# Performance work log

Measured on AMD Instinct MI355X. Metric: run time of the kernel, lower is better.

## Reference

```python
import jax, jax.numpy as jnp
from jax import lax
import numpy as np

N, BITS, NCLS = 2048, 64, 100
LAMBDA = 1.0
ALPHA = 1.0


def setup_inputs() -> dict:
    key = jax.random.key(0)
    ku, kl = jax.random.split(key)
    u = jax.random.normal(ku, (N, BITS), dtype=jnp.float32)
    labels = jax.random.randint(kl, (N,), 0, NCLS)
    y = jax.nn.one_hot(labels, NCLS, dtype=jnp.float32)  # [N, C]
    return {"u": u, "y": y}


def reference(u, y):
    # inner_product[i, j] = <u_i, u_j>;  s[i, j] = (y_i . y_j > 0)
    ip = u @ u.T                      # [N, N]
    s = (y @ y.T) > 0                 # [N, N] bool

    def step(carry, xs):
        tot, cnt = carry
        ip_row, s_row = xs            # [N], [N]
        pos = s_row
        neg = ~s_row
        # triple[p, n] = ip[p] - ip[n] - ALPHA, clamped like the original
        T = jnp.clip(ip_row[:, None] - ip_row[None, :] - ALPHA, -100.0, 50.0)
        # -(T - log(1 + exp(T))) = softplus(T) - T
        L = jax.nn.softplus(T) - T    # [N, N]
        pm = (pos[:, None] & neg[None, :]).astype(L.dtype)
        npairs = pm.sum()
        valid = (pos.sum() > 0) & (neg.sum() > 0)
        row_loss = jnp.where(valid, (L * pm).sum() / jnp.maximum(npairs, 1.0), 0.0)
        return (tot + row_loss, cnt + valid.astype(jnp.float32)), None

    (tot, cnt), _ = lax.scan(step, (jnp.float32(0.0), jnp.float32(0.0)), (ip, s))
    loss1 = jnp.where(cnt > 0, tot / jnp.maximum(cnt, 1.0), 0.0)
    loss2 = LAMBDA * jnp.mean((u - jnp.sign(u)) ** 2)
    return loss1 + loss2
```

## Files before the change

kernel.cpp:

```cpp
#include <hip/hip_runtime.h>
#include <hip/hip_bf16.h>
#include <math.h>

#define NROWS 2048
#define BITS  64
#define NCLS  100
#define ALPHA_C  1.0f
#define LAMBDA_C 1.0f
#define ECLAMP   1.0e9f
#define NPMAX    64
#define EPS      20
#define NCHUNK   32

typedef __bf16 bf16x8 __attribute__((ext_vector_type(8)));
typedef float  floatx4 __attribute__((ext_vector_type(4)));


__device__ __forceinline__ float block_reduce_sum(float v, float* wsum) {
    __syncthreads();
    #pragma unroll
    for (int off = 32; off > 0; off >>= 1) v += __shfl_down(v, off);
    int tid = threadIdx.x;
    if ((tid & 63) == 0) wsum[tid >> 6] = v;
    __syncthreads();
    float r = 0.f;
    if (tid == 0) {
        #pragma unroll
        for (int w = 0; w < 4; ++w) r += wsum[w];
    }
    return r;
}

__device__ __forceinline__ float softplus_mt(float T) {
    return fmaxf(-T, 0.f) + __logf(1.f + __expf(-fabsf(T)));
}


__global__ __launch_bounds__(256) void prep_kernel(const float* __restrict__ u,
                                                   const float* __restrict__ y,
                                                   unsigned short* __restrict__ ub,
                                                   unsigned char* __restrict__ lab8,
                                                   float* __restrict__ qp,
                                                   float* __restrict__ rl,
                                                   unsigned int* __restrict__ done) {
    const int tid = threadIdx.x;
    if (blockIdx.x < 64) {
        __shared__ float wsum[4];
        const int base = blockIdx.x * 2048 + tid * 8;
        float4 v0 = *(const float4*)(u + base);
        float4 v1 = *(const float4*)(u + base + 4);
        float vv[8] = {v0.x, v0.y, v0.z, v0.w, v1.x, v1.y, v1.z, v1.w};
        unsigned short ob[8];
        float q = 0.f;
        #pragma unroll
        for (int m = 0; m < 8; ++m) {
            const float v = vv[m];
            const float sg = (v > 0.f) ? 1.f : ((v < 0.f) ? -1.f : 0.f);
            const float d = v - sg;
            q = fmaf(d, d, q);
            __hip_bfloat16 h = __float2bfloat16(v);
            ob[m] = *reinterpret_cast<unsigned short*>(&h);
        }
        *(uint4*)(ub + base) = *(const uint4*)ob;
        float t = block_reduce_sum(q, wsum);
        if (tid == 0) qp[blockIdx.x] = t;
    } else {
        const int bi = blockIdx.x - 64;
        if (bi == 0 && tid == 0) *done = 0u;
        if (tid == 0) ((float4*)rl)[bi] = make_float4(0.f, 0.f, 0.f, 0.f);
        const int row = bi * 4 + (tid >> 6);
        const int lane = tid & 63;
        const float* yr = y + (size_t)row * NCLS;
        float v0 = yr[lane];
        float v1 = (lane < NCLS - 64) ? yr[lane + 64] : 0.f;
        unsigned long long m0 = __ballot(v0 > 0.5f);
        unsigned long long m1 = __ballot(v1 > 0.5f);
        if (lane == 0) {
            int c = m0 ? (__ffsll(m0) - 1) : (m1 ? 64 + __ffsll(m1) - 1 : 0);
            lab8[row] = (unsigned char)c;
        }
    }
}

__global__ __launch_bounds__(512, 4) void fused_kernel(const float* __restrict__ u,
                                                       const unsigned short* __restrict__ ub,
                                                       const unsigned char* __restrict__ lab8,
                                                       const float* __restrict__ qp,
                                                       float* __restrict__ rl,
                                                       unsigned int* __restrict__ done,
                                                       float* __restrict__ out) {
    __shared__ unsigned char labL[NROWS];
    __shared__ float uloc[16][BITS];
    __shared__ float epT[NPMAX][EPS];
    __shared__ int   clsIdx[NROWS];
    __shared__ int   whist[NCHUNK][NCLS];
    __shared__ int   ccnt[NCLS];
    __shared__ int   cofs[NCLS];
    __shared__ int   np16[16];
    __shared__ float wsum[16][8];
    __shared__ float red8[8];
    __shared__ int   lastflag;

    const int tid  = threadIdx.x;
    const int wave = tid >> 6;
    const int lane = tid & 63;
    const int rsel = lane & 15;
    const int quad = lane >> 4;
    const int koff = quad * 8;
    const int i0    = (blockIdx.x >> 2) * 16;
    const int jbase = (blockIdx.x & 3) * 512;

    ((unsigned int*)labL)[tid] = ((const unsigned int*)lab8)[tid];
    {
        int* wf = &whist[0][0];
        #pragma unroll
        for (int k = 0; k < 7; ++k) {
            const int idx = tid + k * 512;
            if (idx < NCHUNK * NCLS) wf[idx] = 0;
        }
    }
    __syncthreads();

    int rk[4], rc[4];
    const unsigned long long below = (1ull << lane) - 1ull;
    #pragma unroll
    for (int s = 0; s < 4; ++s) {
        const int t = wave * 4 + s;
        const int c = labL[t * 64 + lane];
        unsigned long long m = ~0ull;
        #pragma unroll
        for (int b = 0; b < 7; ++b) {
            const unsigned long long bb = __ballot((c >> b) & 1);
            m &= ((c >> b) & 1) ? bb : ~bb;
        }
        rk[s] = (int)__popcll(m & below);
        rc[s] = c;
        whist[t][c] = (int)__popcll(m);
    }
    __syncthreads();

    if (tid < NCLS) {
        int run = 0;
        #pragma unroll
        for (int t = 0; t < NCHUNK; ++t) {
            const int v = whist[t][tid];
            whist[t][tid] = run;
            run += v;
        }
        ccnt[tid] = run;
    }
    __syncthreads();

    if (tid < 64) {
        const int c0 = (tid < 50) ? ccnt[2 * tid] : 0;
        const int c1 = (tid < 50) ? ccnt[2 * tid + 1] : 0;
        int p = c0 + c1;
        #pragma unroll
        for (int off = 1; off < 64; off <<= 1) {
            const int n = __shfl_up(p, off);
            if (tid >= off) p += n;
        }
        const int excl = p - (c0 + c1);
        if (tid < 50) { cofs[2 * tid] = excl; cofs[2 * tid + 1] = excl + c0; }
    }
    __syncthreads();

    #pragma unroll
    for (int s = 0; s < 4; ++s) {
        const int t = wave * 4 + s;
        const int c = rc[s];
        clsIdx[cofs[c] + whist[t][c] + rk[s]] = t * 64 + lane;
    }
    __syncthreads();

    {
        const int gr = tid >> 5;
        const int gp = tid & 31;
        const int grow = clsIdx[i0 + gr];
        ((float2*)&uloc[gr][0])[gp] =
            ((const float2*)(u + (size_t)grow * BITS))[gp];
    }
    const int arow = clsIdx[i0 + rsel];
    uint4 a0r = *(const uint4*)(ub + (size_t)arow * BITS + koff);
    uint4 a1r = *(const uint4*)(ub + (size_t)arow * BITS + 32 + koff);

    #pragma unroll
    for (int s2 = 0; s2 < 2; ++s2) {
        const int r16 = wave * 2 + s2;
        const int ci  = labL[clsIdx[i0 + r16]];
        const int np  = ccnt[ci];
        const int base = cofs[ci];
        const int npc = (np < NPMAX) ? np : NPMAX;
        float val = 0.f;
        if (lane < npc) {
            const int j = clsIdx[base + lane];
            const float4* uj4 = (const float4*)(u + (size_t)j * BITS);
            const float4* ui4 = (const float4*)(&uloc[r16][0]);
            float s0 = 0.f, s1 = 0.f, s2v = 0.f, s3 = 0.f;
            #pragma unroll
            for (int kk = 0; kk < BITS / 4; ++kk) {
                float4 vj = uj4[kk];
                float4 vi = ui4[kk];
                s0 = fmaf(vj.x, vi.x, s0);
                s1 = fmaf(vj.y, vi.y, s1);
                s2v = fmaf(vj.z, vi.z, s2v);
                s3 = fmaf(vj.w, vi.w, s3);
            }
            val = fminf(__expf(-((s0 + s1) + (s2v + s3))), ECLAMP);
        }
        epT[lane][r16] = val;
        if (lane == 0) np16[r16] = np;
    }

    int rlabq[4];
    #pragma unroll
    for (int r = 0; r < 4; ++r) rlabq[r] = labL[clsIdx[i0 + 4 * quad + r]];

    const bf16x8 A0 = __builtin_bit_cast(bf16x8, a0r);
    const bf16x8 A1 = __builtin_bit_cast(bf16x8, a1r);
    float Eb[4][4];
    #pragma unroll
    for (int t = 0; t < 4; ++t) {
        const int jr = jbase + (wave * 4 + t) * 16 + rsel;
        uint4 b0r = *(const uint4*)(ub + (size_t)jr * BITS + koff);
        uint4 b1r = *(const uint4*)(ub + (size_t)jr * BITS + 32 + koff);
        bf16x8 B0 = __builtin_bit_cast(bf16x8, b0r);
        bf16x8 B1 = __builtin_bit_cast(bf16x8, b1r);
        floatx4 cacc = {0.f, 0.f, 0.f, 0.f};
        cacc = __builtin_amdgcn_mfma_f32_16x16x32_bf16(A0, B0, cacc, 0, 0, 0);
        cacc = __builtin_amdgcn_mfma_f32_16x16x32_bf16(A1, B1, cacc, 0, 0, 0);
        const int colLab = labL[jr];
        #pragma unroll
        for (int r = 0; r < 4; ++r) {
            Eb[t][r] = (colLab == rlabq[r]) ? 0.f
                                            : fminf(__expf(cacc[r] + ALPHA_C), ECLAMP);
        }
    }
    __syncthreads();

    int npmx = 0;
    #pragma unroll
    for (int r = 0; r < 16; ++r) {
        int n = np16[r]; n = (n > NPMAX) ? NPMAX : n;
        npmx = (n > npmx) ? n : npmx;
    }
    const int npr4 = (npmx + 3) & ~3;

    const float SC = 0x1p-60f;
    float mprod[4] = {1.f, 1.f, 1.f, 1.f};
    int   eacc[4]  = {0, 0, 0, 0};
    for (int k = 0; k < npr4; k += 4) {
        const float4 e0 = *(const float4*)(&epT[k][4 * quad]);
        const float4 e1 = *(const float4*)(&epT[k + 1][4 * quad]);
        const float4 e2 = *(const float4*)(&epT[k + 2][4 * quad]);
        const float4 e3 = *(const float4*)(&epT[k + 3][4 * quad]);
        const float e0c[4] = {e0.x * SC, e0.y * SC, e0.z * SC, e0.w * SC};
        const float e1v[4] = {e1.x, e1.y, e1.z, e1.w};
        const float e2c[4] = {e2.x * SC, e2.y * SC, e2.z * SC, e2.w * SC};
        const float e3v[4] = {e3.x, e3.y, e3.z, e3.w};
        #pragma unroll
        for (int t = 0; t < 4; ++t) {
            #pragma unroll
            for (int r = 0; r < 4; ++r) {
                const float q0 = Eb[t][r];
                const float f0 = fmaf(q0, e0c[r], SC);
                const float f1 = fmaf(q0, e1v[r], 1.f);
                const float f2 = fmaf(q0, e2c[r], SC);
                const float f3 = fmaf(q0, e3v[r], 1.f);
                const float P  = (f0 * f1) * (f2 * f3);
                const unsigned int pb = __builtin_bit_cast(unsigned int, P);
                eacc[r] += (int)(pb >> 23);
                const float m = __builtin_bit_cast(float,
                                    (pb & 0x007FFFFFu) | 0x3F800000u);
                mprod[r] *= m;
            }
        }
    }
    const float nadj = 7.0f * (float)npr4;
    float s[4];
    #pragma unroll
    for (int r = 0; r < 4; ++r)
        s[r] = ((float)eacc[r] - nadj) + __log2f(mprod[r]);

    #pragma unroll
    for (int r = 0; r < 4; ++r) {
        #pragma unroll
        for (int off = 1; off < 16; off <<= 1) s[r] += __shfl_xor(s[r], off);
    }
    if (rsel == 0) {
        #pragma unroll
        for (int r = 0; r < 4; ++r) wsum[4 * quad + r][wave] = s[r];
    }
    __syncthreads();
    if (tid < 16) {
        const float ln2 = 0.6931471805599453f;
        const float tot = (((wsum[tid][0] + wsum[tid][1]) +
                            (wsum[tid][2] + wsum[tid][3])) +
                           ((wsum[tid][4] + wsum[tid][5]) +
                            (wsum[tid][6] + wsum[tid][7]))) * ln2;
        atomicAdd(&rl[clsIdx[i0 + tid]], tot);
    }
    __syncthreads();

    if (tid == 0) {
        __threadfence();
        const unsigned int old = atomicAdd(done, 1u);
        lastflag = (old == 511u) ? 1 : 0;
    }
    __syncthreads();
    if (lastflag) {
        float tsum = 0.f, vsum = 0.f;
        for (int row = tid; row < NROWS; row += 512) {
            const float rv = atomicAdd(&rl[row], 0.0f);
            const int np = ccnt[labL[row]];
            const int nn = NROWS - np;
            const int valid = (np > 0 && nn > 0) ? 1 : 0;
            tsum += valid ? (rv / fmaxf((float)np * (float)nn, 1.f)) : 0.f;
            vsum += (float)valid;
        }
        float q = (tid < 64) ? qp[tid] : 0.f;

        float vals[3] = {tsum, vsum, q};
        float outv[3];
        #pragma unroll
        for (int m = 0; m < 3; ++m) {
            float v = vals[m];
            #pragma unroll
            for (int off = 32; off > 0; off >>= 1) v += __shfl_down(v, off);
            if (lane == 0) red8[wave] = v;
            __syncthreads();
            float r = 0.f;
            if (tid == 0) {
                #pragma unroll
                for (int w = 0; w < 8; ++w) r += red8[w];
            }
            __syncthreads();
            outv[m] = r;
        }
        if (tid == 0) {
            const float loss1 = (outv[1] > 0.f) ? (outv[0] / fmaxf(outv[1], 1.f)) : 0.f;
            const float loss2 = LAMBDA_C * (outv[2] / (float)(NROWS * BITS));
            out[0] = loss1 + loss2;
        }
    }
}


__global__ __launch_bounds__(256) void labels_only_kernel(const float* __restrict__ y,
                                                          int* __restrict__ labels) {
    const int tid = threadIdx.x;
    const int row = blockIdx.x * 4 + (tid >> 6);
    const int lane = tid & 63;
    const float* yr = y + (size_t)row * NCLS;
    float v0 = yr[lane];
    float v1 = (lane < NCLS - 64) ? yr[lane + 64] : 0.f;
    unsigned long long m0 = __ballot(v0 > 0.5f);
    unsigned long long m1 = __ballot(v1 > 0.5f);
    if (lane == 0) {
        int c = m0 ? (__ffsll(m0) - 1) : (m1 ? 64 + __ffsll(m1) - 1 : 0);
        labels[row] = c;
    }
}

__global__ __launch_bounds__(256) void row_loss_kernel(const float* __restrict__ u,
                                                       const int* __restrict__ labels,
                                                       float* __restrict__ acc) {
    __shared__ float a[NROWS];
    __shared__ float apv[NROWS];
    __shared__ int lab[NROWS];
    __shared__ float ui[BITS];
    __shared__ int npos_s;
    __shared__ float wsum[4];

    const int i = blockIdx.x;
    const int tid = threadIdx.x;

    if (tid < BITS) ui[tid] = u[(size_t)i * BITS + tid];
    if (tid == 0) npos_s = 0;
    __syncthreads();

    #pragma unroll
    for (int m = 0; m < NROWS / 256; ++m) {
        const int j = tid + m * 256;
        const float4* uj = (const float4*)(u + (size_t)j * BITS);
        float s0 = 0.f, s1 = 0.f, s2 = 0.f, s3 = 0.f;
        #pragma unroll
        for (int q = 0; q < BITS / 4; ++q) {
            float4 v = uj[q];
            s0 = fmaf(v.x, ui[4 * q + 0], s0);
            s1 = fmaf(v.y, ui[4 * q + 1], s1);
            s2 = fmaf(v.z, ui[4 * q + 2], s2);
            s3 = fmaf(v.w, ui[4 * q + 3], s3);
        }
        a[j] = (s0 + s1) + (s2 + s3);
        lab[j] = labels[j];
    }
    __syncthreads();

    const int c = lab[i];
    #pragma unroll
    for (int m = 0; m < NROWS / 256; ++m) {
        const int j = tid + m * 256;
        if (lab[j] == c) { int k = atomicAdd(&npos_s, 1); apv[k] = a[j]; }
    }
    __syncthreads();
    const int npos = npos_s;
    const int nneg = NROWS - npos;

    float b[NROWS / 256];
    #pragma unroll
    for (int m = 0; m < NROWS / 256; ++m) {
        const int j = tid + m * 256;
        b[m] = (lab[j] != c) ? (a[j] + ALPHA_C) : -3.0e38f;
    }

    float lsum = 0.f;
    for (int k = 0; k < npos; ++k) {
        const float apk = apv[k];
        #pragma unroll
        for (int m = 0; m < NROWS / 256; ++m) lsum += softplus_mt(apk - b[m]);
    }

    float tot = block_reduce_sum(lsum, wsum);
    if (tid == 0) {
        const int valid = (npos > 0 && nneg > 0) ? 1 : 0;
        const float npairs = fmaxf((float)npos * (float)nneg, 1.f);
        const float rlv = valid ? (tot / npairs) : 0.f;
        atomicAdd(&acc[0], rlv);
        atomicAdd(&acc[1], (float)valid);
    }
}

__global__ __launch_bounds__(256) void quant_kernel(const float* __restrict__ u,
                                                    float* __restrict__ acc) {
    __shared__ float wsum[4];
    const int stride = gridDim.x * 256;
    float s = 0.f;
    for (int t = blockIdx.x * 256 + threadIdx.x; t < NROWS * BITS; t += stride) {
        float v = u[t];
        float sg = (v > 0.f) ? 1.f : ((v < 0.f) ? -1.f : 0.f);
        float d = v - sg;
        s = fmaf(d, d, s);
    }
    float tot = block_reduce_sum(s, wsum);
    if (threadIdx.x == 0) atomicAdd(&acc[2], tot);
}

__global__ void finalize_kernel(const float* __restrict__ acc,
                                float* __restrict__ out) {
    const float tot = acc[0], cnt = acc[1], q = acc[2];
    const float loss1 = (cnt > 0.f) ? (tot / fmaxf(cnt, 1.f)) : 0.f;
    const float loss2 = LAMBDA_C * (q / (float)(NROWS * BITS));
    out[0] = loss1 + loss2;
}


extern "C" void kernel_launch(void* const* d_in, const int* in_sizes, int n_in,
                              void* d_out, int out_size, void* d_ws, size_t ws_size,
                              hipStream_t stream) {
    const float* u = (const float*)d_in[0];
    const float* y = (const float*)d_in[1];
    float* out = (float*)d_out;

    unsigned char* lab8 = (unsigned char*)d_ws;
    unsigned int* done = (unsigned int*)((char*)d_ws + 4096);
    float* rl = (float*)((char*)d_ws + 8192);
    float* qp = (float*)((char*)d_ws + 16384);
    unsigned short* ub = (unsigned short*)((char*)d_ws + 24576);
    const size_t NEED = 24576 + (size_t)NROWS * BITS * sizeof(unsigned short);

    if (ws_size >= NEED) {
        prep_kernel<<<576, 256, 0, stream>>>(u, y, ub, lab8, qp, rl, done);
        fused_kernel<<<512, 512, 0, stream>>>(u, ub, lab8, qp, rl, done, out);
    } else {
        float* acc2 = (float*)d_ws;
        int*   lab2 = (int*)((char*)d_ws + 256);
        hipMemsetAsync(d_ws, 0, 256, stream);
        labels_only_kernel<<<512, 256, 0, stream>>>(y, lab2);
        row_loss_kernel<<<NROWS, 256, 0, stream>>>(u, lab2, acc2);
        quant_kernel<<<64, 256, 0, stream>>>(u, acc2);
        finalize_kernel<<<1, 1, 0, stream>>>(acc2, out);
    }
}
```

Measured before the change: 82.67 us.

## Hoist per-block class counting sort into a single separate sort kernel

Every fused block used to recompute the class histogram, prefix sums and sorted row index on its own. That work now runs once in a new single-block sortk_kernel, which writes a 16-bit sorted index plus class counts and offsets to workspace. The fused kernel just loads these into shared memory, which shrinks its LDS footprint and prologue. The cost is an extra kernel launch and a serial one-block step between prep and the fused kernel; the class-count scan is also reworked into parallel shuffle scans.

```diff
diff --git a/kernel.cpp b/kernel.cpp
--- a/kernel.cpp
+++ b/kernel.cpp
@@ -82,20 +82,105 @@
     }
 }
 
+__global__ __launch_bounds__(512) void sortk_kernel(const unsigned char* __restrict__ lab8,
+                                                    unsigned short* __restrict__ clsIdxG,
+                                                    int* __restrict__ ccntG,
+                                                    int* __restrict__ cofsG) {
+    __shared__ unsigned char labL[NROWS];
+    __shared__ int whist[NCHUNK][NCLS];
+    __shared__ int ccnt[NCLS];
+    __shared__ int cofs[NCLS];
+
+    const int tid  = threadIdx.x;
+    const int wave = tid >> 6;
+    const int lane = tid & 63;
+
+    ((unsigned int*)labL)[tid] = ((const unsigned int*)lab8)[tid];
+    {
+        int* wf = &whist[0][0];
+        #pragma unroll
+        for (int k = 0; k < 7; ++k) {
+            const int idx = tid + k * 512;
+            if (idx < NCHUNK * NCLS) wf[idx] = 0;
+        }
+    }
+    __syncthreads();
+
+    int rk[4], rc[4];
+    const unsigned long long below = (1ull << lane) - 1ull;
+    #pragma unroll
+    for (int s = 0; s < 4; ++s) {
+        const int t = wave * 4 + s;
+        const int c = labL[t * 64 + lane];
+        unsigned long long m = ~0ull;
+        #pragma unroll
+        for (int b = 0; b < 7; ++b) {
+            const unsigned long long bb = __ballot((c >> b) & 1);
+            m &= ((c >> b) & 1) ? bb : ~bb;
+        }
+        rk[s] = (int)__popcll(m & below);
+        rc[s] = c;
+        whist[t][c] = (int)__popcll(m);
+    }
+    __syncthreads();
+
+    #pragma unroll
+    for (int p = 0; p < 7; ++p) {
+        const int cls = p * 16 + (tid >> 5);
+        const int ch  = tid & 31;
+        if (cls < NCLS) {
+            const int v = whist[ch][cls];
+            int x = v;
+            #pragma unroll
+            for (int off = 1; off < 32; off <<= 1) {
+                const int n = __shfl_up(x, off, 32);
+                if (ch >= off) x += n;
+            }
+            whist[ch][cls] = x - v;
+            if (ch == 31) ccnt[cls] = x;
+        }
+    }
+    __syncthreads();
+
+    if (tid < 64) {
+        const int c0 = (tid < 50) ? ccnt[2 * tid] : 0;
+        const int c1 = (tid < 50) ? ccnt[2 * tid + 1] : 0;
+        int p = c0 + c1;
+        #pragma unroll
+        for (int off = 1; off < 64; off <<= 1) {
+            const int n = __shfl_up(p, off);
+            if (tid >= off) p += n;
+        }
+        const int excl = p - (c0 + c1);
+        if (tid < 50) { cofs[2 * tid] = excl; cofs[2 * tid + 1] = excl + c0; }
+    }
+    __syncthreads();
+
+    #pragma unroll
+    for (int s = 0; s < 4; ++s) {
+        const int t = wave * 4 + s;
+        const int c = rc[s];
+        clsIdxG[cofs[c] + whist[t][c] + rk[s]] = (unsigned short)(t * 64 + lane);
+    }
+    if (tid < NCLS) { ccntG[tid] = ccnt[tid]; cofsG[tid] = cofs[tid]; }
+}
+
 __global__ __launch_bounds__(512, 4) void fused_kernel(const float* __restrict__ u,
                                                        const unsigned short* __restrict__ ub,
                                                        const unsigned char* __restrict__ lab8,
+                                                       const unsigned short* __restrict__ clsIdxG,
+                                                       const int* __restrict__ ccntG,
+                                                       const int* __restrict__ cofsG,
                                                        const float* __restrict__ qp,
                                                        float* __restrict__ rl,
                                                        unsigned int* __restrict__ done,
                                                        float* __restrict__ out) {
     __shared__ unsigned char labL[NROWS];
+    __shared__ unsigned short clsL[NROWS];
     __shared__ float uloc[16][BITS];
     __shared__ float epT[NPMAX][EPS];
-    __shared__ int   clsIdx[NROWS];
-    __shared__ int   whist[NCHUNK][NCLS];
-    __shared__ int   ccnt[NCLS];
-    __shared__ int   cofs[NCLS];
+    __shared__ int   ccntL[NCLS];
+    __shared__ int   cofsL[NCLS];
     __shared__ int   np16[16];
     __shared__ float wsum[16][8];
     __shared__ float red8[8];
@@ -111,89 +196,31 @@
     const int jbase = (blockIdx.x & 3) * 512;
 
     ((unsigned int*)labL)[tid] = ((const unsigned int*)lab8)[tid];
-    {
-        int* wf = &whist[0][0];
-        #pragma unroll
-        for (int k = 0; k < 7; ++k) {
-            const int idx = tid + k * 512;
-            if (idx < NCHUNK * NCLS) wf[idx] = 0;
-        }
-    }
-    __syncthreads();
-
-    int rk[4], rc[4];
-    const unsigned long long below = (1ull << lane) - 1ull;
-    #pragma unroll
-    for (int s = 0; s < 4; ++s) {
-        const int t = wave * 4 + s;
-        const int c = labL[t * 64 + lane];
-        unsigned long long m = ~0ull;
-        #pragma unroll
-        for (int b = 0; b < 7; ++b) {
-            const unsigned long long bb = __ballot((c >> b) & 1);
-            m &= ((c >> b) & 1) ? bb : ~bb;
-        }
-        rk[s] = (int)__popcll(m & below);
-        rc[s] = c;
-        whist[t][c] = (int)__popcll(m);
-    }
-    __syncthreads();
-
-    if (tid < NCLS) {
-        int run = 0;
-        #pragma unroll
-        for (int t = 0; t < NCHUNK; ++t) {
-            const int v = whist[t][tid];
-            whist[t][tid] = run;
-            run += v;
-        }
-        ccnt[tid] = run;
-    }
-    __syncthreads();
-
-    if (tid < 64) {
-        const int c0 = (tid < 50) ? ccnt[2 * tid] : 0;
-        const int c1 = (tid < 50) ? ccnt[2 * tid + 1] : 0;
-        int p = c0 + c1;
-        #pragma unroll
-        for (int off = 1; off < 64; off <<= 1) {
-            const int n = __shfl_up(p, off);
-            if (tid >= off) p += n;
-        }
-        const int excl = p - (c0 + c1);
-        if (tid < 50) { cofs[2 * tid] = excl; cofs[2 * tid + 1] = excl + c0; }
-    }
-    __syncthreads();
-
-    #pragma unroll
-    for (int s = 0; s < 4; ++s) {
-        const int t = wave * 4 + s;
-        const int c = rc[s];
-        clsIdx[cofs[c] + whist[t][c] + rk[s]] = t * 64 + lane;
-    }
+    ((uint2*)clsL)[tid] = ((const uint2*)clsIdxG)[tid];
+    if (tid < NCLS) { ccntL[tid] = ccntG[tid]; cofsL[tid] = cofsG[tid]; }
     __syncthreads();
 
     {
         const int gr = tid >> 5;
         const int gp = tid & 31;
-        const int grow = clsIdx[i0 + gr];
+        const int grow = clsL[i0 + gr];
         ((float2*)&uloc[gr][0])[gp] =
             ((const float2*)(u + (size_t)grow * BITS))[gp];
     }
-    const int arow = clsIdx[i0 + rsel];
+    const int arow = clsL[i0 + rsel];
     uint4 a0r = *(const uint4*)(ub + (size_t)arow * BITS + koff);
     uint4 a1r = *(const uint4*)(ub + (size_t)arow * BITS + 32 + koff);
 
     #pragma unroll
     for (int s2 = 0; s2 < 2; ++s2) {
         const int r16 = wave * 2 + s2;
-        const int ci  = labL[clsIdx[i0 + r16]];
-        const int np  = ccnt[ci];
-        const int base = cofs[ci];
+        const int ci  = labL[clsL[i0 + r16]];
+        const int np  = ccntL[ci];
+        const int base = cofsL[ci];
         const int npc = (np < NPMAX) ? np : NPMAX;
         float val = 0.f;
         if (lane < npc) {
-            const int j = clsIdx[base + lane];
+            const int j = clsL[base + lane];
             const float4* uj4 = (const float4*)(u + (size_t)j * BITS);
             const float4* ui4 = (const float4*)(&uloc[r16][0]);
             float s0 = 0.f, s1 = 0.f, s2v = 0.f, s3 = 0.f;
@@ -214,7 +241,7 @@
 
     int rlabq[4];
     #pragma unroll
-    for (int r = 0; r < 4; ++r) rlabq[r] = labL[clsIdx[i0 + 4 * quad + r]];
+    for (int r = 0; r < 4; ++r) rlabq[r] = labL[clsL[i0 + 4 * quad + r]];
 
     const bf16x8 A0 = __builtin_bit_cast(bf16x8, a0r);
     const bf16x8 A1 = __builtin_bit_cast(bf16x8, a1r);
@@ -298,7 +325,7 @@
                             (wsum[tid][2] + wsum[tid][3])) +
                            ((wsum[tid][4] + wsum[tid][5]) +
                             (wsum[tid][6] + wsum[tid][7]))) * ln2;
-        atomicAdd(&rl[clsIdx[i0 + tid]], tot);
+        atomicAdd(&rl[clsL[i0 + tid]], tot);
     }
     __syncthreads();
 
@@ -312,7 +339,7 @@
         float tsum = 0.f, vsum = 0.f;
         for (int row = tid; row < NROWS; row += 512) {
             const float rv = atomicAdd(&rl[row], 0.0f);
-            const int np = ccnt[labL[row]];
+            const int np = ccntL[labL[row]];
             const int nn = NROWS - np;
             const int valid = (np > 0 && nn > 0) ? 1 : 0;
             tsum += valid ? (rv / fmaxf((float)np * (float)nn, 1.f)) : 0.f;
@@ -466,12 +493,17 @@
     unsigned int* done = (unsigned int*)((char*)d_ws + 4096);
     float* rl = (float*)((char*)d_ws + 8192);
     float* qp = (float*)((char*)d_ws + 16384);
+    unsigned short* clsIdxG = (unsigned short*)((char*)d_ws + 18432);
+    int* ccntG = (int*)((char*)d_ws + 22528);
+    int* cofsG = (int*)((char*)d_ws + 23040);
     unsigned short* ub = (unsigned short*)((char*)d_ws + 24576);
     const size_t NEED = 24576 + (size_t)NROWS * BITS * sizeof(unsigned short);
 
     if (ws_size >= NEED) {
         prep_kernel<<<576, 256, 0, stream>>>(u, y, ub, lab8, qp, rl, done);
-        fused_kernel<<<512, 512, 0, stream>>>(u, ub, lab8, qp, rl, done, out);
+        sortk_kernel<<<1, 512, 0, stream>>>(lab8, clsIdxG, ccntG, cofsG);
+        fused_kernel<<<512, 512, 0, stream>>>(u, ub, lab8, clsIdxG, ccntG, cofsG,
+                                              qp, rl, done, out);
     } else {
         float* acc2 = (float*)d_ws;
         int*   lab2 = (int*)((char*)d_ws + 256);
```

Result: slower. 87.02 us (+5.3%).
